# Kernel tuning notes

Measured on AMD Instinct MI355X. Metric: run time of the kernel, lower is better.

Reference implementation:

```python
import jax, jax.numpy as jnp
import numpy as np

# ---- module hyperparameters ----
B, L, F = 128, 720, 128
SEG = 24            # segment_length
NSEG = L // SEG     # 30 input segments
WIN = 15            # window_size
NPRED = 96 // SEG   # 4 prediction segments
D = 128             # encode_dim
H = 512             # hidden_dim
DECAY = 0.9
C = 1.0             # curvature
EPS = 1e-6
MAXN = 1.0 - 1e-5   # max radius of Poincare ball (c=1)
SQC = 1.0           # sqrt(C)

# ---- Poincare-ball manifold ops ----
def _sqnorm(x):
    return jnp.sum(x * x, axis=-1, keepdims=True)

def _norm(x):
    return jnp.sqrt(jnp.maximum(_sqnorm(x), EPS * EPS))

def _project(x):
    n = _norm(x)
    return jnp.where(n > MAXN, x * (MAXN / n), x)

def _artanh(x):
    return jnp.arctanh(jnp.clip(x, -1.0 + 1e-7, 1.0 - 1e-7))

def mobius_add(x, y):
    xy = jnp.sum(x * y, axis=-1, keepdims=True)
    x2, y2 = _sqnorm(x), _sqnorm(y)
    num = (1.0 + 2.0 * C * xy + C * y2) * x + (1.0 - C * x2) * y
    den = 1.0 + 2.0 * C * xy + C * C * x2 * y2
    return num / jnp.maximum(den, EPS)

def expmap0(v):
    n = _norm(v)
    return _project(jnp.tanh(SQC * n) * v / (SQC * n))

def logmap0(y):
    n = _norm(y)
    return _artanh(SQC * n) * y / (SQC * n)

def expmap(x, v):
    lam = 2.0 / jnp.maximum(1.0 - C * _sqnorm(x), EPS)
    n = _norm(v)
    second = jnp.tanh(SQC * lam * n / 2.0) * v / (SQC * n)
    return _project(mobius_add(x, second))

def logmap(x, y):
    d = mobius_add(-x, y)
    n = _norm(d)
    lam = 2.0 / jnp.maximum(1.0 - C * _sqnorm(x), EPS)
    return (2.0 / (SQC * lam)) * _artanh(SQC * n) * d / n


def setup_inputs() -> dict:
    key = jax.random.key(0)
    ks = jax.random.split(key, 12)
    s = 0.05
    return {
        'trend':           0.5 * jax.random.normal(ks[0], (B, L, F), jnp.float32),
        'seasonal_coarse': 0.5 * jax.random.normal(ks[1], (B, L, F), jnp.float32),
        'seasonal_fine':   0.5 * jax.random.normal(ks[2], (B, L, F), jnp.float32),
        'residual':        0.5 * jax.random.normal(ks[3], (B, L, F), jnp.float32),
        'W_t': s * jax.random.normal(ks[4], (SEG, D), jnp.float32), 'b_t': jnp.zeros((D,), jnp.float32),
        'W_c': s * jax.random.normal(ks[5], (SEG, D), jnp.float32), 'b_c': jnp.zeros((D,), jnp.float32),
        'W_f': s * jax.random.normal(ks[6], (SEG, D), jnp.float32), 'b_f': jnp.zeros((D,), jnp.float32),
        'W_r': s * jax.random.normal(ks[7], (SEG, D), jnp.float32), 'b_r': jnp.zeros((D,), jnp.float32),
        'alpha': jnp.array([0.5], jnp.float32),
        'W1': s * jax.random.normal(ks[8], (D, H), jnp.float32), 'b1': jnp.zeros((H,), jnp.float32),
        'W2': s * jax.random.normal(ks[9], (H, SEG), jnp.float32), 'b2': jnp.zeros((SEG,), jnp.float32),
    }


def reference(trend, seasonal_coarse, seasonal_fine, residual,
              W_t, b_t, W_c, b_c, W_f, b_f, W_r, b_r,
              alpha, W1, b1, W2, b2):
    b, l, f = trend.shape

    def collapse(x):  # [B,L,F] -> [B*F, NSEG, SEG]
        return x.transpose(0, 2, 1).reshape(b * f, NSEG, SEG)

    t_s, c_s, f_s, r_s = map(collapse, (trend, seasonal_coarse, seasonal_fine, residual))

    # per-segment tangent encoding (channel-independent, shared params)
    tan = (jnp.einsum('bns,sd->bnd', t_s, W_t) + b_t
           + jnp.einsum('bns,sd->bnd', c_s, W_c) + b_c
           + jnp.einsum('bns,sd->bnd', f_s, W_f) + b_f
           + jnp.einsum('bns,sd->bnd', r_s, W_r) + b_r)
    z = expmap0(tan)                     # [BF, NSEG, D] on the ball
    z_cur = z[:, -WIN:, :]

    idx = jnp.arange(WIN - 1, dtype=jnp.float32)
    w = DECAY ** (WIN - 2 - idx)
    w = w / w.sum()

    preds, latents = [], []
    for _ in range(NPRED):
        z_last = z_cur[:, -1]
        vel = logmap(z_cur[:, :-1], z_cur[:, 1:])
        avg_v = jnp.sum(vel * w[None, :, None], axis=1)    # [BF, D]
        z_next = expmap(z_last, alpha * avg_v)             # dynamics step
        latents.append(z_next)
        # reconstruction head: logmap0 -> MLP -> segment
        t0 = logmap0(z_next)
        seg = jax.nn.relu(t0 @ W1 + b1) @ W2 + b2          # [BF, SEG]
        preds.append(seg)
        z_cur = jnp.concatenate([z_cur[:, 1:], z_next[:, None]], axis=1)

    p = jnp.stack(preds, axis=1).reshape(b * f, NPRED * SEG)
    predictions = p.reshape(b, f, NPRED * SEG).transpose(0, 2, 1)  # [B, pred_len, F]
    return predictions
```

## Files before the change

kernel.cpp:

```cpp
#include <hip/hip_runtime.h>
#include <hip/hip_bf16.h>

namespace {
constexpr int kL = 720, kF = 128;
constexpr int kWin = 15;
constexpr float kEps = 1e-6f;
constexpr float kMaxN = 1.0f - 1e-5f;
constexpr int kT0off = 360;
constexpr int ZTR = 132;
constexpr int AROW = 104;
constexpr int XR = 129;
constexpr size_t kOffT0   = 0;
constexpr size_t kOffW1   = 16777216;
constexpr size_t kOffW2   = kOffW1 + 131072;
constexpr size_t kOffBt   = kOffW2 + 32768;
constexpr size_t kOffBsum = kOffBt + 73728;
constexpr size_t kOffZ2   = 17018880;
constexpr size_t kOffZ    = 18874368;
constexpr size_t kWsNew   = kOffZ + 125829120;
}

typedef float f32x4 __attribute__((ext_vector_type(4)));
typedef short s16x8 __attribute__((ext_vector_type(8)));

__device__ __forceinline__ float rcp_f(float x) { return __builtin_amdgcn_rcpf(x); }
__device__ __forceinline__ float sqrt_f(float x) { return __builtin_amdgcn_sqrtf(x); }
__device__ __forceinline__ float tanh_f(float x) {
  float t = __builtin_amdgcn_exp2f(x * -2.8853900817779268f);
  return (1.0f - t) * rcp_f(1.0f + t);
}
__device__ __forceinline__ float artanh_f(float n) {
  float nc = fminf(n, 1.0f - 1e-7f);
  return 0.34657359027997264f * __builtin_amdgcn_logf((1.0f + nc) * rcp_f(1.0f - nc));
}

template<int CTRL>
__device__ __forceinline__ float dpp_add(float v) {
  int mv = __builtin_amdgcn_update_dpp(0, __float_as_int(v), CTRL, 0xF, 0xF, false);
  return v + __int_as_float(mv);
}
__device__ __forceinline__ float sum16(float v) {
  v = dpp_add<0xB1>(v);
  v = dpp_add<0x4E>(v);
  v = dpp_add<0x141>(v);
  v = dpp_add<0x128>(v);
  return v;
}
__device__ __forceinline__ float sum64(float v) {
  v = sum16(v);
  v += __shfl_xor(v, 16);
  v += __shfl_xor(v, 32);
  return v;
}
__device__ __forceinline__ float rlane(float v, int i) {
  return __int_as_float(__builtin_amdgcn_readlane(__float_as_int(v), i));
}
__device__ __forceinline__ unsigned short rne_bf16(float f, float& fval) {
  unsigned u = __float_as_uint(f);
  unsigned r = (u + 0x7FFFu + ((u >> 16) & 1u)) & 0xFFFF0000u;
  fval = __uint_as_float(r);
  return (unsigned short)(r >> 16);
}

extern "C" __global__ __launch_bounds__(256)
void mwhf_prep(const float* __restrict__ W1, const float* __restrict__ W2,
               const float* __restrict__ W_t, const float* __restrict__ W_c,
               const float* __restrict__ W_f, const float* __restrict__ W_r,
               const float* __restrict__ b_t, const float* __restrict__ b_c,
               const float* __restrict__ b_f, const float* __restrict__ b_r,
               __hip_bfloat16* __restrict__ W1bf, __hip_bfloat16* __restrict__ W2bf,
               __hip_bfloat16* __restrict__ BtH, __hip_bfloat16* __restrict__ BtM,
               __hip_bfloat16* __restrict__ BtL, float* __restrict__ bsum)
{
  const int b = blockIdx.x, tid = threadIdx.x;
  if (b < 64) {
    const int n0 = b * 8;
    for (int e = tid; e < 1024; e += 256) {
      int n_l = e & 7, k = e >> 3;
      W1bf[(size_t)(n0 + n_l) * 128 + k] = __float2bfloat16(W1[(size_t)k * 512 + n0 + n_l]);
    }
  } else if (b < 68) {
    const int k0 = (b - 64) * 128;
    for (int e = tid; e < 4096; e += 256) {
      int p = e >> 7, k_l = e & 127;
      float v = (p < 24) ? W2[(size_t)(k0 + k_l) * 24 + p] : 0.0f;
      W2bf[(size_t)p * 512 + k0 + k_l] = __float2bfloat16(v);
    }
  } else if (b < 72) {
    const int st = b - 68;
    const float* src = (st == 0) ? W_t : (st == 1) ? W_c : (st == 2) ? W_f : W_r;
    for (int e = tid; e < 3072; e += 256) {
      int s = e >> 7, d = e & 127;
      float x = src[e];
      __hip_bfloat16 h = __float2bfloat16(x);
      float r1 = x - __bfloat162float(h);
      __hip_bfloat16 m = __float2bfloat16(r1);
      float r2 = r1 - __bfloat162float(m);
      const int o = d * 96 + st * 24 + s;
      BtH[o] = h;
      BtM[o] = m;
      BtL[o] = __float2bfloat16(r2);
    }
  } else {
    if (tid < 128) bsum[tid] = b_t[tid] + b_c[tid] + b_f[tid] + b_r[tid];
  }
}

extern "C" __global__ __launch_bounds__(256, 3)
void mwhf_k1a2(const float* __restrict__ trend,
               const float* __restrict__ seas_c,
               const float* __restrict__ seas_f,
               const float* __restrict__ resid,
               const __hip_bfloat16* __restrict__ BtH,
               const __hip_bfloat16* __restrict__ BtM,
               const __hip_bfloat16* __restrict__ BtL,
               const float* __restrict__ bsum,
               float* __restrict__ z_ws, float* __restrict__ z2_ws)
{
  __shared__ __align__(16) float X[96 * XR];

  const int tid = threadIdx.x;
  const int seg = blockIdx.x;
  const int bb  = blockIdx.y;

  {
    const float* ptrs[4] = {trend, seas_c, seas_f, resid};
#pragma unroll
    for (int it = 0; it < 12; ++it) {
      int e = it * 256 + tid;
      int row = e >> 5;
      int fq = (e & 31) * 4;
      int st = row / 24, sI = row - st * 24;
      float4 v = *(const float4*)&ptrs[st][(size_t)(bb * kL + kT0off + seg * 24 + sI) * kF + fq];
      float* dst = &X[row * XR + fq];
      dst[0] = v.x; dst[1] = v.y; dst[2] = v.z; dst[3] = v.w;
    }
  }
  __syncthreads();

  const int w = tid >> 6, lane = tid & 63;
  const int l16 = lane & 15, quad = lane >> 4;
  const int fbase = w * 32;

  f32x4 acc[2][8];
#pragma unroll
  for (int s = 0; s < 2; ++s)
#pragma unroll
    for (int t = 0; t < 8; ++t) acc[s][t] = (f32x4)0.f;

  const __hip_bfloat16* bhp = BtH + l16 * 96 + quad * 8;
  const __hip_bfloat16* bmp = BtM + l16 * 96 + quad * 8;
  const __hip_bfloat16* blp = BtL + l16 * 96 + quad * 8;

#pragma unroll
  for (int ks = 0; ks < 3; ++ks) {
    s16x8 ah[2], am[2], al[2];
#pragma unroll
    for (int s = 0; s < 2; ++s) {
      const int f = fbase + s * 16 + l16;
      const float* ar = &X[(ks * 32 + quad * 8) * XR + f];
#pragma unroll
      for (int j = 0; j < 8; ++j) {
        float x = ar[j * XR];
        unsigned hu = __float_as_uint(x) & 0xFFFF0000u;
        float r1 = x - __uint_as_float(hu);
        float mf; unsigned short mb = rne_bf16(r1, mf);
        float r2 = r1 - mf;
        float lf; unsigned short lb = rne_bf16(r2, lf);
        (void)lf;
        ah[s][j] = (short)(hu >> 16);
        am[s][j] = (short)mb;
        al[s][j] = (short)lb;
      }
    }
#pragma unroll
    for (int t = 0; t < 8; ++t) {
      s16x8 bh = *(const s16x8*)(bhp + t * 1536 + ks * 32);
      s16x8 bm = *(const s16x8*)(bmp + t * 1536 + ks * 32);
      s16x8 bl = *(const s16x8*)(blp + t * 1536 + ks * 32);
#pragma unroll
      for (int s = 0; s < 2; ++s) {
        acc[s][t] = __builtin_amdgcn_mfma_f32_16x16x32_bf16(ah[s], bh, acc[s][t], 0, 0, 0);
        acc[s][t] = __builtin_amdgcn_mfma_f32_16x16x32_bf16(am[s], bh, acc[s][t], 0, 0, 0);
        acc[s][t] = __builtin_amdgcn_mfma_f32_16x16x32_bf16(ah[s], bm, acc[s][t], 0, 0, 0);
        acc[s][t] = __builtin_amdgcn_mfma_f32_16x16x32_bf16(al[s], bh, acc[s][t], 0, 0, 0);
        acc[s][t] = __builtin_amdgcn_mfma_f32_16x16x32_bf16(ah[s], bl, acc[s][t], 0, 0, 0);
        acc[s][t] = __builtin_amdgcn_mfma_f32_16x16x32_bf16(am[s], bm, acc[s][t], 0, 0, 0);
      }
    }
  }

  float part[2][4] = {{0.f,0.f,0.f,0.f},{0.f,0.f,0.f,0.f}};
#pragma unroll
  for (int t = 0; t < 8; ++t) {
    float bv = bsum[t * 16 + l16];
#pragma unroll
    for (int s = 0; s < 2; ++s)
#pragma unroll
      for (int r = 0; r < 4; ++r) {
        float v = acc[s][t][r] + bv;
        acc[s][t][r] = v;
        part[s][r] += v * v;
      }
  }
#pragma unroll
  for (int s = 0; s < 2; ++s)
#pragma unroll
    for (int r = 0; r < 4; ++r) part[s][r] = sum16(part[s][r]);

#pragma unroll
  for (int s = 0; s < 2; ++s)
#pragma unroll
    for (int r = 0; r < 4; ++r) {
      const int f = fbase + s * 16 + quad * 4 + r;
      float v2 = part[s][r];
      float nv = sqrt_f(fmaxf(v2, 1e-12f));
      float sc = tanh_f(nv) * rcp_f(nv);
      float y2 = sc * sc * v2;
      float yn = sqrt_f(fmaxf(y2, 1e-12f));
      float proj = (yn > kMaxN) ? (kMaxN * rcp_f(yn)) : 1.0f;
      float scl = sc * proj;
      float* zr = z_ws + (size_t)(bb * 128 + f) * 1920 + seg * 128;
#pragma unroll
      for (int t = 0; t < 8; ++t)
        zr[t * 16 + l16] = acc[s][t][r] * scl;
      if (l16 == 0) z2_ws[(bb * 128 + f) * 16 + seg] = y2 * proj * proj;
    }
}

extern "C" __global__ __launch_bounds__(256, 6)
void mwhf_k1b(const float* __restrict__ z_ws, const float* __restrict__ z2_ws,
              const float* __restrict__ alpha,
              __hip_bfloat16* __restrict__ t0_out)
{
  __shared__ float z2s[80];
  __shared__ float pds[80];
  const int tid = threadIdx.x;
  const int w = tid >> 6, l = tid & 63;
  const int ro = blockIdx.x * 4 + w;

  float zx[19], zy[19];
  const float* zr = z_ws + (size_t)ro * 1920;
#pragma unroll
  for (int j = 0; j < 15; ++j) {
    float2 v = *(const float2*)&zr[j * 128 + 2 * l];
    zx[j] = v.x; zy[j] = v.y;
  }
  if (l < 15) z2s[w * 20 + l] = z2_ws[ro * 16 + l];

  {
    float pd[14];
#pragma unroll
    for (int j = 0; j < 14; ++j) pd[j] = zx[j] * zx[j + 1] + zy[j] * zy[j + 1];
#pragma unroll
    for (int j = 0; j < 14; ++j) pd[j] = sum64(pd[j]);
    if (l == 0) {
#pragma unroll
      for (int j = 0; j < 14; ++j) pds[w * 20 + j] = pd[j];
    }
  }

  const float alp = alpha[0];
  const float cw14 = (l < 14)
      ? __builtin_amdgcn_exp2f((float)(13 - l) * -0.15200309344504997f) * 0.12966260f
      : 0.f;

#pragma unroll
  for (int it = 0; it < 4; ++it) {
    float cA = 0.f, cB = 0.f, cW = 0.f;
    if (l < 14) {
      float dp = pds[w * 20 + it + l];
      float x2 = z2s[w * 20 + it + l];
      float y2 = z2s[w * 20 + it + l + 1];
      cA = 1.f - 2.f * dp + y2;
      cB = 1.f - x2;
      float den = fmaxf(1.f - 2.f * dp + x2 * y2, kEps);
      float invd = rcp_f(den);
      float d2 = (cA * cA * x2 - 2.f * cA * cB * dp + cB * cB * y2) * (invd * invd);
      float n = sqrt_f(fmaxf(d2, 1e-12f));
      float coef = fmaxf(cB, kEps) * artanh_f(n) * rcp_f(n);
      cW = cw14 * coef * invd;
    }
    float avx = 0.f, avy = 0.f;
#pragma unroll
    for (int i = 0; i < 14; ++i) {
      float sA = rlane(cA, i), sB = rlane(cB, i), sW = rlane(cW, i);
      float tx = sB * zx[it + i + 1] - sA * zx[it + i];
      float ty = sB * zy[it + i + 1] - sA * zy[it + i];
      avx += sW * tx;
      avy += sW * ty;
    }
    float vx = alp * avx, vy = alp * avy;
    const int pl = it + 14;
    float x2l = z2s[w * 20 + pl];
    float v2 = vx * vx + vy * vy;
    float xdv = zx[pl] * vx + zy[pl] * vy;
    v2 = sum64(v2);
    xdv = sum64(xdv);
    float nv = sqrt_f(fmaxf(v2, 1e-12f));
    float lam = 2.f * rcp_f(fmaxf(1.f - x2l, kEps));
    float co = tanh_f(0.5f * lam * nv) * rcp_f(nv);
    float s2 = co * co * v2;
    float xy = co * xdv;
    float P = 1.f + 2.f * xy + s2;
    float Q = 1.f - x2l;
    float den2 = fmaxf(1.f + 2.f * xy + x2l * s2, kEps);
    float invd2 = rcp_f(den2);
    float znx = (P * zx[pl] + Q * co * vx) * invd2;
    float zny = (P * zy[pl] + Q * co * vy) * invd2;
    float zn2 = (P * P * x2l + 2.f * P * Q * xy + Q * Q * s2) * (invd2 * invd2);
    float pdn = (P * x2l + Q * xy) * invd2;
    float yn = sqrt_f(fmaxf(zn2, 1e-12f));
    float proj = (yn > kMaxN) ? (kMaxN * rcp_f(yn)) : 1.f;
    znx *= proj; zny *= proj;
    zn2 *= proj * proj;
    pdn *= proj;
    zx[15 + it] = znx; zy[15 + it] = zny;
    if (l == 0) {
      z2s[w * 20 + 15 + it] = zn2;
      pds[w * 20 + 14 + it] = pdn;
    }
    float n0 = sqrt_f(fmaxf(zn2, 1e-12f));
    float fac = artanh_f(n0) * rcp_f(n0);
    __hip_bfloat162 hv;
    hv.x = __float2bfloat16(fac * znx);
    hv.y = __float2bfloat16(fac * zny);
    *(__hip_bfloat162*)(t0_out + ((size_t)ro * 4 + it) * 128 + 2 * l) = hv;
  }
}

extern "C" __global__ __launch_bounds__(256, 4)
void mwhf_k1(const float* __restrict__ trend,
             const float* __restrict__ seas_c,
             const float* __restrict__ seas_f,
             const float* __restrict__ resid,
             const __hip_bfloat16* __restrict__ BtH,
             const __hip_bfloat16* __restrict__ BtM,
             const __hip_bfloat16* __restrict__ BtL,
             const float* __restrict__ bsum,
             const float* __restrict__ alpha,
             __hip_bfloat16* __restrict__ t0_out)
{
  __shared__ __align__(16) char smem_raw[3 * 64 * AROW * 2];
  __shared__ float z2s[80];
  __shared__ float pds[80];

  float* ublk = (float*)smem_raw;
  __hip_bfloat16* Ah = (__hip_bfloat16*)smem_raw;
  __hip_bfloat16* Am = Ah + 64 * AROW;
  __hip_bfloat16* Al = Am + 64 * AROW;

  const int tid = threadIdx.x;
  const int bix = blockIdx.x;
  const int bb = (bix & 7) * 16 + (bix >> 8);
  const int f0 = ((bix >> 3) & 31) * 4;
  const int row0 = bb * 128 + f0;

  for (int e = tid; e < 192; e += 256) {
    int rr = e / 48, cc = e - rr * 48;
    int off = (rr * 16 + 15) * AROW;
    ((unsigned int*)(Ah + off))[cc] = 0u;
    ((unsigned int*)(Am + off))[cc] = 0u;
    ((unsigned int*)(Al + off))[cc] = 0u;
  }
  {
    const float* ptrs[4] = {trend, seas_c, seas_f, resid};
    for (int e = tid; e < 1440; e += 256) {
      int seg = e / 96;
      int k = e - seg * 96;
      int st = k / 24, s = k - st * 24;
      const float* p = ptrs[st];
      float4 v = *(const float4*)&p[(size_t)(bb * kL + kT0off + seg * 24 + s) * kF + f0];
      float xv[4] = {v.x, v.y, v.z, v.w};
#pragma unroll
      for (int f = 0; f < 4; ++f) {
        int m = f * 16 + seg;
        __hip_bfloat16 h = __float2bfloat16(xv[f]);
        float r1 = xv[f] - __bfloat162float(h);
        __hip_bfloat16 mm = __float2bfloat16(r1);
        float r2 = r1 - __bfloat162float(mm);
        Ah[m * AROW + k] = h;
        Am[m * AROW + k] = mm;
        Al[m * AROW + k] = __float2bfloat16(r2);
      }
    }
  }
  __syncthreads();

  const int w = tid >> 6;
  const int lane = tid & 63;
  const int l16 = lane & 15, quad = lane >> 4;

  f32x4 acc0[8];
  float scale4[4], zz4[4];
  {
    s16x8 ah[3], am[3], al[3];
    const int abase = (w * 16 + l16) * AROW + quad * 8;
#pragma unroll
    for (int ks = 0; ks < 3; ++ks) {
      ah[ks] = *(const s16x8*)(Ah + abase + ks * 32);
      am[ks] = *(const s16x8*)(Am + abase + ks * 32);
      al[ks] = *(const s16x8*)(Al + abase + ks * 32);
    }
#pragma unroll
    for (int t = 0; t < 8; ++t) acc0[t] = (f32x4)0.f;
    const __hip_bfloat16* bhp = BtH + l16 * 96 + quad * 8;
    const __hip_bfloat16* bmp = BtM + l16 * 96 + quad * 8;
    const __hip_bfloat16* blp = BtL + l16 * 96 + quad * 8;
#pragma unroll
    for (int t = 0; t < 8; ++t) {
#pragma unroll
      for (int ks = 0; ks < 3; ++ks) {
        s16x8 bh = *(const s16x8*)(bhp + t * 1536 + ks * 32);
        s16x8 bm = *(const s16x8*)(bmp + t * 1536 + ks * 32);
        s16x8 bl = *(const s16x8*)(blp + t * 1536 + ks * 32);
        acc0[t] = __builtin_amdgcn_mfma_f32_16x16x32_bf16(ah[ks], bh, acc0[t], 0, 0, 0);
        acc0[t] = __builtin_amdgcn_mfma_f32_16x16x32_bf16(am[ks], bh, acc0[t], 0, 0, 0);
        acc0[t] = __builtin_amdgcn_mfma_f32_16x16x32_bf16(ah[ks], bm, acc0[t], 0, 0, 0);
        acc0[t] = __builtin_amdgcn_mfma_f32_16x16x32_bf16(al[ks], bh, acc0[t], 0, 0, 0);
        acc0[t] = __builtin_amdgcn_mfma_f32_16x16x32_bf16(ah[ks], bl, acc0[t], 0, 0, 0);
        acc0[t] = __builtin_amdgcn_mfma_f32_16x16x32_bf16(am[ks], bm, acc0[t], 0, 0, 0);
      }
    }
    float part[4] = {0.f, 0.f, 0.f, 0.f};
#pragma unroll
    for (int t = 0; t < 8; ++t) {
      float bv = bsum[t * 16 + l16];
#pragma unroll
      for (int r = 0; r < 4; ++r) {
        float v = acc0[t][r] + bv;
        acc0[t][r] = v;
        part[r] += v * v;
      }
    }
#pragma unroll
    for (int r = 0; r < 4; ++r) part[r] = sum16(part[r]);
#pragma unroll
    for (int r = 0; r < 4; ++r) {
      float v2 = part[r];
      float nv = sqrt_f(fmaxf(v2, 1e-12f));
      float sc = tanh_f(nv) * rcp_f(nv);
      float y2 = sc * sc * v2;
      float yn = sqrt_f(fmaxf(y2, 1e-12f));
      float proj = (yn > kMaxN) ? (kMaxN * rcp_f(yn)) : 1.0f;
      scale4[r] = sc * proj;
      zz4[r] = y2 * proj * proj;
    }
  }
  __syncthreads();
  {
#pragma unroll
    for (int r = 0; r < 4; ++r) {
      int row = quad * 4 + r;
      if (row < kWin) {
#pragma unroll
        for (int t = 0; t < 8; ++t)
          ublk[(w * kWin + row) * ZTR + t * 16 + l16] = acc0[t][r] * scale4[r];
        if (l16 == 0) z2s[w * 20 + row] = zz4[r];
      }
    }
  }
  __syncthreads();

  {
    const int l = lane;
    float zx[19], zy[19];
#pragma unroll
    for (int j = 0; j < 15; ++j) {
      float2 v = *(const float2*)&ublk[(w * kWin + j) * ZTR + 2 * l];
      zx[j] = v.x; zy[j] = v.y;
    }
    {
      float pd[14];
#pragma unroll
      for (int j = 0; j < 14; ++j) pd[j] = zx[j] * zx[j + 1] + zy[j] * zy[j + 1];
#pragma unroll
      for (int j = 0; j < 14; ++j) pd[j] = sum64(pd[j]);
      if (l == 0) {
#pragma unroll
        for (int j = 0; j < 14; ++j) pds[w * 20 + j] = pd[j];
      }
    }
    const float alp = alpha[0];
    const float cw14 = (l < 14)
        ? __builtin_amdgcn_exp2f((float)(13 - l) * -0.15200309344504997f) * 0.12966260f
        : 0.f;
#pragma unroll
    for (int it = 0; it < 4; ++it) {
      float cA = 0.f, cB = 0.f, cW = 0.f;
      if (l < 14) {
        float dp = pds[w * 20 + it + l];
        float x2 = z2s[w * 20 + it + l];
        float y2 = z2s[w * 20 + it + l + 1];
        cA = 1.f - 2.f * dp + y2;
        cB = 1.f - x2;
        float den = fmaxf(1.f - 2.f * dp + x2 * y2, kEps);
        float invd = rcp_f(den);
        float d2 = (cA * cA * x2 - 2.f * cA * cB * dp + cB * cB * y2) * (invd * invd);
        float n = sqrt_f(fmaxf(d2, 1e-12f));
        float coef = fmaxf(cB, kEps) * artanh_f(n) * rcp_f(n);
        cW = cw14 * coef * invd;
      }
      float avx = 0.f, avy = 0.f;
#pragma unroll
      for (int i = 0; i < 14; ++i) {
        float sA = rlane(cA, i), sB = rlane(cB, i), sW = rlane(cW, i);
        float tx = sB * zx[it + i + 1] - sA * zx[it + i];
        float ty = sB * zy[it + i + 1] - sA * zy[it + i];
        avx += sW * tx;
        avy += sW * ty;
      }
      float vx = alp * avx, vy = alp * avy;
      const int pl = it + 14;
      float x2l = z2s[w * 20 + pl];
      float v2 = vx * vx + vy * vy;
      float xdv = zx[pl] * vx + zy[pl] * vy;
      v2 = sum64(v2);
      xdv = sum64(xdv);
      float nv = sqrt_f(fmaxf(v2, 1e-12f));
      float lam = 2.f * rcp_f(fmaxf(1.f - x2l, kEps));
      float co = tanh_f(0.5f * lam * nv) * rcp_f(nv);
      float s2 = co * co * v2;
      float xy = co * xdv;
      float P = 1.f + 2.f * xy + s2;
      float Q = 1.f - x2l;
      float den2 = fmaxf(1.f + 2.f * xy + x2l * s2, kEps);
      float invd2 = rcp_f(den2);
      float znx = (P * zx[pl] + Q * co * vx) * invd2;
      float zny = (P * zy[pl] + Q * co * vy) * invd2;
      float zn2 = (P * P * x2l + 2.f * P * Q * xy + Q * Q * s2) * (invd2 * invd2);
      float pdn = (P * x2l + Q * xy) * invd2;
      float yn = sqrt_f(fmaxf(zn2, 1e-12f));
      float proj = (yn > kMaxN) ? (kMaxN * rcp_f(yn)) : 1.f;
      znx *= proj; zny *= proj;
      zn2 *= proj * proj;
      pdn *= proj;
      zx[15 + it] = znx; zy[15 + it] = zny;
      if (l == 0) {
        z2s[w * 20 + 15 + it] = zn2;
        pds[w * 20 + 14 + it] = pdn;
      }
      float n0 = sqrt_f(fmaxf(zn2, 1e-12f));
      float fac = artanh_f(n0) * rcp_f(n0);
      __hip_bfloat162 hv;
      hv.x = __float2bfloat16(fac * znx);
      hv.y = __float2bfloat16(fac * zny);
      *(__hip_bfloat162*)(t0_out + ((size_t)(row0 + w) * 4 + it) * 128 + 2 * l) = hv;
    }
  }
}

extern "C" __global__ __launch_bounds__(256, 4)
void mwhf_k2g(const __hip_bfloat16* __restrict__ t0g,
              const __hip_bfloat16* __restrict__ W1bf,
              const __hip_bfloat16* __restrict__ W2bf,
              const float* __restrict__ b1, const float* __restrict__ b2,
              float* __restrict__ outp)
{
  __shared__ __align__(16) __hip_bfloat16 hids[32 * 512];
  s16x8* hidv = (s16x8*)hids;

  const int tid = threadIdx.x;
  const int w = tid >> 6, lane = tid & 63;
  const int l16 = lane & 15, quad = lane >> 4;
  const int mbase = blockIdx.x * 32;
  const int ng = w * 128;

  s16x8 afr[2][4];
#pragma unroll
  for (int s = 0; s < 2; ++s)
#pragma unroll
    for (int kc = 0; kc < 4; ++kc)
      afr[s][kc] = *(const s16x8*)(t0g + (size_t)(mbase + s * 16 + l16) * 128 + kc * 32 + quad * 8);

  f32x4 acc[2][8];
#pragma unroll
  for (int s = 0; s < 2; ++s)
#pragma unroll
    for (int t = 0; t < 8; ++t) acc[s][t] = (f32x4)0.f;

#pragma unroll
  for (int t = 0; t < 8; ++t) {
    const __hip_bfloat16* bp = W1bf + (size_t)(ng + t * 16 + l16) * 128 + quad * 8;
#pragma unroll
    for (int kc = 0; kc < 4; ++kc) {
      s16x8 bfr = *(const s16x8*)(bp + kc * 32);
      acc[0][t] = __builtin_amdgcn_mfma_f32_16x16x32_bf16(afr[0][kc], bfr, acc[0][t], 0, 0, 0);
      acc[1][t] = __builtin_amdgcn_mfma_f32_16x16x32_bf16(afr[1][kc], bfr, acc[1][t], 0, 0, 0);
    }
  }
#pragma unroll
  for (int t = 0; t < 8; ++t) {
    const int nl = ng + t * 16 + l16;
    float bv = b1[nl];
#pragma unroll
    for (int s = 0; s < 2; ++s)
#pragma unroll
      for (int r = 0; r < 4; ++r) {
        int m = s * 16 + quad * 4 + r;
// ... 14 lines not shown
      a2 = __builtin_amdgcn_mfma_f32_16x16x32_bf16(av, bfr, a2, 0, 0, 0);
    }
    const int p = t2 * 16 + l16;
    if (p < 24) {
      float bv = b2[p];
#pragma unroll
      for (int r = 0; r < 4; ++r) {
        int m = mbase + s2i * 16 + quad * 4 + r;
        int bbi = m >> 9, it = m & 3, f = (m >> 2) & 127;
        outp[(size_t)bbi * 12288 + (it * 24 + p) * 128 + f] = a2[r] + bv;
      }
    }
  }
}

extern "C" void kernel_launch(void* const* d_in, const int* in_sizes, int n_in,
                              void* d_out, int out_size, void* d_ws, size_t ws_size,
                              hipStream_t stream) {
  (void)in_sizes; (void)n_in; (void)out_size;
  const float* trend = (const float*)d_in[0];
  const float* sc    = (const float*)d_in[1];
  const float* sf    = (const float*)d_in[2];
  const float* rs    = (const float*)d_in[3];
  const float* W_t   = (const float*)d_in[4];
  const float* b_t   = (const float*)d_in[5];
  const float* W_c   = (const float*)d_in[6];
  const float* b_c   = (const float*)d_in[7];
  const float* W_f   = (const float*)d_in[8];
  const float* b_f   = (const float*)d_in[9];
  const float* W_r   = (const float*)d_in[10];
  const float* b_r   = (const float*)d_in[11];
  const float* alpha = (const float*)d_in[12];
  const float* W1    = (const float*)d_in[13];
  const float* b1    = (const float*)d_in[14];
  const float* W2    = (const float*)d_in[15];
  const float* b2    = (const float*)d_in[16];

  char* ws = (char*)d_ws;
  __hip_bfloat16* t0   = (__hip_bfloat16*)(ws + kOffT0);
  __hip_bfloat16* W1bf = (__hip_bfloat16*)(ws + kOffW1);
  __hip_bfloat16* W2bf = (__hip_bfloat16*)(ws + kOffW2);
  __hip_bfloat16* BtH  = (__hip_bfloat16*)(ws + kOffBt);
  __hip_bfloat16* BtM  = BtH + 12288;
  __hip_bfloat16* BtL  = BtM + 12288;
  float* bsum = (float*)(ws + kOffBsum);
  float* z2w  = (float*)(ws + kOffZ2);
  float* zw   = (float*)(ws + kOffZ);
  float* outp = (float*)d_out;

  hipLaunchKernelGGL(mwhf_prep, dim3(73), dim3(256), 0, stream,
                     W1, W2, W_t, W_c, W_f, W_r, b_t, b_c, b_f, b_r,
                     W1bf, W2bf, BtH, BtM, BtL, bsum);
  if (ws_size >= kWsNew) {
    hipLaunchKernelGGL(mwhf_k1a2, dim3(15, 128), dim3(256), 0, stream,
                       trend, sc, sf, rs, BtH, BtM, BtL, bsum, zw, z2w);
    hipLaunchKernelGGL(mwhf_k1b, dim3(4096), dim3(256), 0, stream,
                       zw, z2w, alpha, t0);
  } else {
    hipLaunchKernelGGL(mwhf_k1, dim3(4096), dim3(256), 0, stream,
                       trend, sc, sf, rs, BtH, BtM, BtL, bsum, alpha, t0);
  }
  hipLaunchKernelGGL(mwhf_k2g, dim3(2048), dim3(256), 0, stream,
                     t0, W1bf, W2bf, b1, b2, outp);
}
```

Measured before the change: 374.8 us.

## Fuse dynamics step with MLP head and split encoder blocks by feature half

The dynamics kernel now also runs the reconstruction MLP. It keeps the 32 t0 rows per block in swizzled shared memory, so the t0 round trip through global memory and one kernel launch go away. The encoder kernel is split across feature halves: twice as many blocks, each with half the shared memory and accumulators, and launch bounds raised to allow more blocks per CU. The fused kernel uses 512 threads and more shared memory per block, which may lower occupancy.

```diff
diff --git a/kernel.cpp b/kernel.cpp
--- a/kernel.cpp
+++ b/kernel.cpp
@@ -9,7 +9,7 @@
 constexpr int kT0off = 360;
 constexpr int ZTR = 132;
 constexpr int AROW = 104;
-constexpr int XR = 129;
+constexpr int XR2 = 65;
 constexpr size_t kOffT0   = 0;
 constexpr size_t kOffW1   = 16777216;
 constexpr size_t kOffW2   = kOffW1 + 131072;
@@ -106,8 +106,8 @@
   }
 }
 
-extern "C" __global__ __launch_bounds__(256, 3)
-void mwhf_k1a2(const float* __restrict__ trend,
+extern "C" __global__ __launch_bounds__(256, 4)
+void mwhf_k1a3(const float* __restrict__ trend,
                const float* __restrict__ seas_c,
                const float* __restrict__ seas_f,
                const float* __restrict__ resid,
@@ -117,22 +117,24 @@
                const float* __restrict__ bsum,
                float* __restrict__ z_ws, float* __restrict__ z2_ws)
 {
-  __shared__ __align__(16) float X[96 * XR];
+  __shared__ __align__(16) float X[96 * XR2];
 
   const int tid = threadIdx.x;
   const int seg = blockIdx.x;
-  const int bb  = blockIdx.y;
+  const int bh  = blockIdx.y;
+  const int bb  = bh >> 1;
+  const int fh  = (bh & 1) * 64;
 
   {
     const float* ptrs[4] = {trend, seas_c, seas_f, resid};
 #pragma unroll
-    for (int it = 0; it < 12; ++it) {
+    for (int it = 0; it < 6; ++it) {
       int e = it * 256 + tid;
-      int row = e >> 5;
-      int fq = (e & 31) * 4;
+      int row = e >> 4;
+      int fq = (e & 15) * 4;
       int st = row / 24, sI = row - st * 24;
-      float4 v = *(const float4*)&ptrs[st][(size_t)(bb * kL + kT0off + seg * 24 + sI) * kF + fq];
-      float* dst = &X[row * XR + fq];
+      float4 v = *(const float4*)&ptrs[st][(size_t)(bb * kL + kT0off + seg * 24 + sI) * kF + fh + fq];
+      float* dst = &X[row * XR2 + fq];
       dst[0] = v.x; dst[1] = v.y; dst[2] = v.z; dst[3] = v.w;
     }
   }
@@ -140,13 +142,10 @@
 
   const int w = tid >> 6, lane = tid & 63;
   const int l16 = lane & 15, quad = lane >> 4;
-  const int fbase = w * 32;
-
-  f32x4 acc[2][8];
-#pragma unroll
-  for (int s = 0; s < 2; ++s)
-#pragma unroll
-    for (int t = 0; t < 8; ++t) acc[s][t] = (f32x4)0.f;
+
+  f32x4 acc[8];
+#pragma unroll
+  for (int t = 0; t < 8; ++t) acc[t] = (f32x4)0.f;
 
   const __hip_bfloat16* bhp = BtH + l16 * 96 + quad * 8;
   const __hip_bfloat16* bmp = BtM + l16 * 96 + quad * 8;
@@ -154,322 +153,99 @@
 
 #pragma unroll
   for (int ks = 0; ks < 3; ++ks) {
-    s16x8 ah[2], am[2], al[2];
-#pragma unroll
-    for (int s = 0; s < 2; ++s) {
-      const int f = fbase + s * 16 + l16;
-      const float* ar = &X[(ks * 32 + quad * 8) * XR + f];
+    s16x8 ah, am, al;
+    {
+      const float* ar = &X[(ks * 32 + quad * 8) * XR2 + w * 16 + l16];
 #pragma unroll
       for (int j = 0; j < 8; ++j) {
-        float x = ar[j * XR];
+        float x = ar[j * XR2];
         unsigned hu = __float_as_uint(x) & 0xFFFF0000u;
         float r1 = x - __uint_as_float(hu);
         float mf; unsigned short mb = rne_bf16(r1, mf);
         float r2 = r1 - mf;
         float lf; unsigned short lb = rne_bf16(r2, lf);
         (void)lf;
-        ah[s][j] = (short)(hu >> 16);
-        am[s][j] = (short)mb;
-        al[s][j] = (short)lb;
+        ah[j] = (short)(hu >> 16);
+        am[j] = (short)mb;
+        al[j] = (short)lb;
       }
     }
 #pragma unroll
     for (int t = 0; t < 8; ++t) {
-      s16x8 bh = *(const s16x8*)(bhp + t * 1536 + ks * 32);
-      s16x8 bm = *(const s16x8*)(bmp + t * 1536 + ks * 32);
-      s16x8 bl = *(const s16x8*)(blp + t * 1536 + ks * 32);
-#pragma unroll
-      for (int s = 0; s < 2; ++s) {
-        acc[s][t] = __builtin_amdgcn_mfma_f32_16x16x32_bf16(ah[s], bh, acc[s][t], 0, 0, 0);
-        acc[s][t] = __builtin_amdgcn_mfma_f32_16x16x32_bf16(am[s], bh, acc[s][t], 0, 0, 0);
-        acc[s][t] = __builtin_amdgcn_mfma_f32_16x16x32_bf16(ah[s], bm, acc[s][t], 0, 0, 0);
-        acc[s][t] = __builtin_amdgcn_mfma_f32_16x16x32_bf16(al[s], bh, acc[s][t], 0, 0, 0);
-        acc[s][t] = __builtin_amdgcn_mfma_f32_16x16x32_bf16(ah[s], bl, acc[s][t], 0, 0, 0);
-        acc[s][t] = __builtin_amdgcn_mfma_f32_16x16x32_bf16(am[s], bm, acc[s][t], 0, 0, 0);
-      }
-    }
-  }
-
-  float part[2][4] = {{0.f,0.f,0.f,0.f},{0.f,0.f,0.f,0.f}};
+      s16x8 bhv = *(const s16x8*)(bhp + t * 1536 + ks * 32);
+      s16x8 bmv = *(const s16x8*)(bmp + t * 1536 + ks * 32);
+      s16x8 blv = *(const s16x8*)(blp + t * 1536 + ks * 32);
+      acc[t] = __builtin_amdgcn_mfma_f32_16x16x32_bf16(ah, bhv, acc[t], 0, 0, 0);
+      acc[t] = __builtin_amdgcn_mfma_f32_16x16x32_bf16(am, bhv, acc[t], 0, 0, 0);
+      acc[t] = __builtin_amdgcn_mfma_f32_16x16x32_bf16(ah, bmv, acc[t], 0, 0, 0);
+      acc[t] = __builtin_amdgcn_mfma_f32_16x16x32_bf16(al, bhv, acc[t], 0, 0, 0);
+      acc[t] = __builtin_amdgcn_mfma_f32_16x16x32_bf16(ah, blv, acc[t], 0, 0, 0);
+      acc[t] = __builtin_amdgcn_mfma_f32_16x16x32_bf16(am, bmv, acc[t], 0, 0, 0);
+    }
+  }
+
+  float part[4] = {0.f, 0.f, 0.f, 0.f};
 #pragma unroll
   for (int t = 0; t < 8; ++t) {
     float bv = bsum[t * 16 + l16];
 #pragma unroll
-    for (int s = 0; s < 2; ++s)
-#pragma unroll
-      for (int r = 0; r < 4; ++r) {
-        float v = acc[s][t][r] + bv;
-        acc[s][t][r] = v;
-        part[s][r] += v * v;
-      }
-  }
-#pragma unroll
-  for (int s = 0; s < 2; ++s)
-#pragma unroll
-    for (int r = 0; r < 4; ++r) part[s][r] = sum16(part[s][r]);
-
-#pragma unroll
-  for (int s = 0; s < 2; ++s)
-#pragma unroll
     for (int r = 0; r < 4; ++r) {
-      const int f = fbase + s * 16 + quad * 4 + r;
-      float v2 = part[s][r];
-      float nv = sqrt_f(fmaxf(v2, 1e-12f));
-      float sc = tanh_f(nv) * rcp_f(nv);
-      float y2 = sc * sc * v2;
-      float yn = sqrt_f(fmaxf(y2, 1e-12f));
-      float proj = (yn > kMaxN) ? (kMaxN * rcp_f(yn)) : 1.0f;
-      float scl = sc * proj;
-      float* zr = z_ws + (size_t)(bb * 128 + f) * 1920 + seg * 128;
-#pragma unroll
-      for (int t = 0; t < 8; ++t)
-        zr[t * 16 + l16] = acc[s][t][r] * scl;
-      if (l16 == 0) z2_ws[(bb * 128 + f) * 16 + seg] = y2 * proj * proj;
-    }
-}
-
-extern "C" __global__ __launch_bounds__(256, 6)
-void mwhf_k1b(const float* __restrict__ z_ws, const float* __restrict__ z2_ws,
-              const float* __restrict__ alpha,
-              __hip_bfloat16* __restrict__ t0_out)
+      float v = acc[t][r] + bv;
+      acc[t][r] = v;
+      part[r] += v * v;
+    }
+  }
+#pragma unroll
+  for (int r = 0; r < 4; ++r) part[r] = sum16(part[r]);
+
+#pragma unroll
+  for (int r = 0; r < 4; ++r) {
+    const int row = bh * 64 + w * 16 + quad * 4 + r;
+    float v2 = part[r];
+    float nv = sqrt_f(fmaxf(v2, 1e-12f));
+    float sc = tanh_f(nv) * rcp_f(nv);
+    float y2 = sc * sc * v2;
+    float yn = sqrt_f(fmaxf(y2, 1e-12f));
+    float proj = (yn > kMaxN) ? (kMaxN * rcp_f(yn)) : 1.0f;
+    float scl = sc * proj;
+    float* zr = z_ws + (size_t)row * 1920 + seg * 128;
+#pragma unroll
+    for (int t = 0; t < 8; ++t)
+      zr[t * 16 + l16] = acc[t][r] * scl;
+    if (l16 == 0) z2_ws[row * 16 + seg] = y2 * proj * proj;
+  }
+}
+
+extern "C" __global__ __launch_bounds__(512, 4)
+void mwhf_k1bg(const float* __restrict__ z_ws, const float* __restrict__ z2_ws,
+               const float* __restrict__ alpha,
+               const __hip_bfloat16* __restrict__ W1bf,
+               const __hip_bfloat16* __restrict__ W2bf,
+               const float* __restrict__ b1, const float* __restrict__ b2,
+               float* __restrict__ outp)
 {
-  __shared__ float z2s[80];
-  __shared__ float pds[80];
+  __shared__ __align__(16) __hip_bfloat16 t0s[32 * 128];
+  __shared__ __align__(16) __hip_bfloat16 hids[32 * 512];
+  __shared__ float z2s[160];
+  __shared__ float pds[160];
+  s16x8* hidv = (s16x8*)hids;
+
   const int tid = threadIdx.x;
   const int w = tid >> 6, l = tid & 63;
-  const int ro = blockIdx.x * 4 + w;
-
-  float zx[19], zy[19];
-  const float* zr = z_ws + (size_t)ro * 1920;
-#pragma unroll
-  for (int j = 0; j < 15; ++j) {
-    float2 v = *(const float2*)&zr[j * 128 + 2 * l];
-    zx[j] = v.x; zy[j] = v.y;
-  }
-  if (l < 15) z2s[w * 20 + l] = z2_ws[ro * 16 + l];
+  const int l16 = l & 15, quad = l >> 4;
+  const int mbase = blockIdx.x * 32;
 
   {
-    float pd[14];
-#pragma unroll
-    for (int j = 0; j < 14; ++j) pd[j] = zx[j] * zx[j + 1] + zy[j] * zy[j + 1];
-#pragma unroll
-    for (int j = 0; j < 14; ++j) pd[j] = sum64(pd[j]);
-    if (l == 0) {
-#pragma unroll
-      for (int j = 0; j < 14; ++j) pds[w * 20 + j] = pd[j];
-    }
-  }
-
-  const float alp = alpha[0];
-  const float cw14 = (l < 14)
-      ? __builtin_amdgcn_exp2f((float)(13 - l) * -0.15200309344504997f) * 0.12966260f
-      : 0.f;
-
-#pragma unroll
-  for (int it = 0; it < 4; ++it) {
-    float cA = 0.f, cB = 0.f, cW = 0.f;
-    if (l < 14) {
-      float dp = pds[w * 20 + it + l];
-      float x2 = z2s[w * 20 + it + l];
-      float y2 = z2s[w * 20 + it + l + 1];
-      cA = 1.f - 2.f * dp + y2;
-      cB = 1.f - x2;
-      float den = fmaxf(1.f - 2.f * dp + x2 * y2, kEps);
-      float invd = rcp_f(den);
-      float d2 = (cA * cA * x2 - 2.f * cA * cB * dp + cB * cB * y2) * (invd * invd);
-      float n = sqrt_f(fmaxf(d2, 1e-12f));
-      float coef = fmaxf(cB, kEps) * artanh_f(n) * rcp_f(n);
-      cW = cw14 * coef * invd;
-    }
-    float avx = 0.f, avy = 0.f;
-#pragma unroll
-    for (int i = 0; i < 14; ++i) {
-      float sA = rlane(cA, i), sB = rlane(cB, i), sW = rlane(cW, i);
-      float tx = sB * zx[it + i + 1] - sA * zx[it + i];
-      float ty = sB * zy[it + i + 1] - sA * zy[it + i];
-      avx += sW * tx;
-      avy += sW * ty;
-    }
-    float vx = alp * avx, vy = alp * avy;
-    const int pl = it + 14;
-    float x2l = z2s[w * 20 + pl];
-    float v2 = vx * vx + vy * vy;
-    float xdv = zx[pl] * vx + zy[pl] * vy;
-    v2 = sum64(v2);
-    xdv = sum64(xdv);
-    float nv = sqrt_f(fmaxf(v2, 1e-12f));
-    float lam = 2.f * rcp_f(fmaxf(1.f - x2l, kEps));
-    float co = tanh_f(0.5f * lam * nv) * rcp_f(nv);
-    float s2 = co * co * v2;
-    float xy = co * xdv;
-    float P = 1.f + 2.f * xy + s2;
-    float Q = 1.f - x2l;
-    float den2 = fmaxf(1.f + 2.f * xy + x2l * s2, kEps);
-    float invd2 = rcp_f(den2);
-    float znx = (P * zx[pl] + Q * co * vx) * invd2;
-    float zny = (P * zy[pl] + Q * co * vy) * invd2;
-    float zn2 = (P * P * x2l + 2.f * P * Q * xy + Q * Q * s2) * (invd2 * invd2);
-    float pdn = (P * x2l + Q * xy) * invd2;
-    float yn = sqrt_f(fmaxf(zn2, 1e-12f));
-    float proj = (yn > kMaxN) ? (kMaxN * rcp_f(yn)) : 1.f;
-    znx *= proj; zny *= proj;
-    zn2 *= proj * proj;
-    pdn *= proj;
-    zx[15 + it] = znx; zy[15 + it] = zny;
-    if (l == 0) {
-      z2s[w * 20 + 15 + it] = zn2;
-      pds[w * 20 + 14 + it] = pdn;
-    }
-    float n0 = sqrt_f(fmaxf(zn2, 1e-12f));
-    float fac = artanh_f(n0) * rcp_f(n0);
-    __hip_bfloat162 hv;
-    hv.x = __float2bfloat16(fac * znx);
-    hv.y = __float2bfloat16(fac * zny);
-    *(__hip_bfloat162*)(t0_out + ((size_t)ro * 4 + it) * 128 + 2 * l) = hv;
-  }
-}
-
-extern "C" __global__ __launch_bounds__(256, 4)
-void mwhf_k1(const float* __restrict__ trend,
-             const float* __restrict__ seas_c,
-             const float* __restrict__ seas_f,
-             const float* __restrict__ resid,
-             const __hip_bfloat16* __restrict__ BtH,
-             const __hip_bfloat16* __restrict__ BtM,
-             const __hip_bfloat16* __restrict__ BtL,
-             const float* __restrict__ bsum,
-             const float* __restrict__ alpha,
-             __hip_bfloat16* __restrict__ t0_out)
-{
-  __shared__ __align__(16) char smem_raw[3 * 64 * AROW * 2];
-  __shared__ float z2s[80];
-  __shared__ float pds[80];
-
-  float* ublk = (float*)smem_raw;
-  __hip_bfloat16* Ah = (__hip_bfloat16*)smem_raw;
-  __hip_bfloat16* Am = Ah + 64 * AROW;
-  __hip_bfloat16* Al = Am + 64 * AROW;
-
-  const int tid = threadIdx.x;
-  const int bix = blockIdx.x;
-  const int bb = (bix & 7) * 16 + (bix >> 8);
-  const int f0 = ((bix >> 3) & 31) * 4;
-  const int row0 = bb * 128 + f0;
-
-  for (int e = tid; e < 192; e += 256) {
-    int rr = e / 48, cc = e - rr * 48;
-    int off = (rr * 16 + 15) * AROW;
-    ((unsigned int*)(Ah + off))[cc] = 0u;
-    ((unsigned int*)(Am + off))[cc] = 0u;
-    ((unsigned int*)(Al + off))[cc] = 0u;
-  }
-  {
-    const float* ptrs[4] = {trend, seas_c, seas_f, resid};
-    for (int e = tid; e < 1440; e += 256) {
-      int seg = e / 96;
-      int k = e - seg * 96;
-      int st = k / 24, s = k - st * 24;
-      const float* p = ptrs[st];
-      float4 v = *(const float4*)&p[(size_t)(bb * kL + kT0off + seg * 24 + s) * kF + f0];
-      float xv[4] = {v.x, v.y, v.z, v.w};
-#pragma unroll
-      for (int f = 0; f < 4; ++f) {
-        int m = f * 16 + seg;
-        __hip_bfloat16 h = __float2bfloat16(xv[f]);
-        float r1 = xv[f] - __bfloat162float(h);
-        __hip_bfloat16 mm = __float2bfloat16(r1);
-        float r2 = r1 - __bfloat162float(mm);
-        Ah[m * AROW + k] = h;
-        Am[m * AROW + k] = mm;
-        Al[m * AROW + k] = __float2bfloat16(r2);
-      }
-    }
-  }
-  __syncthreads();
-
-  const int w = tid >> 6;
-  const int lane = tid & 63;
-  const int l16 = lane & 15, quad = lane >> 4;
-
-  f32x4 acc0[8];
-  float scale4[4], zz4[4];
-  {
-    s16x8 ah[3], am[3], al[3];
-    const int abase = (w * 16 + l16) * AROW + quad * 8;
-#pragma unroll
-    for (int ks = 0; ks < 3; ++ks) {
-      ah[ks] = *(const s16x8*)(Ah + abase + ks * 32);
-      am[ks] = *(const s16x8*)(Am + abase + ks * 32);
-      al[ks] = *(const s16x8*)(Al + abase + ks * 32);
-    }
-#pragma unroll
-    for (int t = 0; t < 8; ++t) acc0[t] = (f32x4)0.f;
-    const __hip_bfloat16* bhp = BtH + l16 * 96 + quad * 8;
-    const __hip_bfloat16* bmp = BtM + l16 * 96 + quad * 8;
-    const __hip_bfloat16* blp = BtL + l16 * 96 + quad * 8;
-#pragma unroll
-    for (int t = 0; t < 8; ++t) {
-#pragma unroll
-      for (int ks = 0; ks < 3; ++ks) {
-        s16x8 bh = *(const s16x8*)(bhp + t * 1536 + ks * 32);
-        s16x8 bm = *(const s16x8*)(bmp + t * 1536 + ks * 32);
-        s16x8 bl = *(const s16x8*)(blp + t * 1536 + ks * 32);
-        acc0[t] = __builtin_amdgcn_mfma_f32_16x16x32_bf16(ah[ks], bh, acc0[t], 0, 0, 0);
-        acc0[t] = __builtin_amdgcn_mfma_f32_16x16x32_bf16(am[ks], bh, acc0[t], 0, 0, 0);
-        acc0[t] = __builtin_amdgcn_mfma_f32_16x16x32_bf16(ah[ks], bm, acc0[t], 0, 0, 0);
-        acc0[t] = __builtin_amdgcn_mfma_f32_16x16x32_bf16(al[ks], bh, acc0[t], 0, 0, 0);
-        acc0[t] = __builtin_amdgcn_mfma_f32_16x16x32_bf16(ah[ks], bl, acc0[t], 0, 0, 0);
-        acc0[t] = __builtin_amdgcn_mfma_f32_16x16x32_bf16(am[ks], bm, acc0[t], 0, 0, 0);
-      }
-    }
-    float part[4] = {0.f, 0.f, 0.f, 0.f};
-#pragma unroll
-    for (int t = 0; t < 8; ++t) {
-      float bv = bsum[t * 16 + l16];
-#pragma unroll
-      for (int r = 0; r < 4; ++r) {
-        float v = acc0[t][r] + bv;
-        acc0[t][r] = v;
-        part[r] += v * v;
-      }
-    }
-#pragma unroll
-    for (int r = 0; r < 4; ++r) part[r] = sum16(part[r]);
-#pragma unroll
-    for (int r = 0; r < 4; ++r) {
-      float v2 = part[r];
-      float nv = sqrt_f(fmaxf(v2, 1e-12f));
-      float sc = tanh_f(nv) * rcp_f(nv);
-      float y2 = sc * sc * v2;
-      float yn = sqrt_f(fmaxf(y2, 1e-12f));
-      float proj = (yn > kMaxN) ? (kMaxN * rcp_f(yn)) : 1.0f;
-      scale4[r] = sc * proj;
-      zz4[r] = y2 * proj * proj;
-    }
-  }
-  __syncthreads();
-  {
-#pragma unroll
-    for (int r = 0; r < 4; ++r) {
-      int row = quad * 4 + r;
-      if (row < kWin) {
-#pragma unroll
-        for (int t = 0; t < 8; ++t)
-          ublk[(w * kWin + row) * ZTR + t * 16 + l16] = acc0[t][r] * scale4[r];
-        if (l16 == 0) z2s[w * 20 + row] = zz4[r];
-      }
-    }
-  }
-  __syncthreads();
-
-  {
-    const int l = lane;
+    const int ro = blockIdx.x * 8 + w;
     float zx[19], zy[19];
+    const float* zr = z_ws + (size_t)ro * 1920;
 #pragma unroll
     for (int j = 0; j < 15; ++j) {
-      float2 v = *(const float2*)&ublk[(w * kWin + j) * ZTR + 2 * l];
+      float2 v = *(const float2*)&zr[j * 128 + 2 * l];
       zx[j] = v.x; zy[j] = v.y;
     }
+    if (l < 15) z2s[w * 20 + l] = z2_ws[ro * 16 + l];
+
     {
       float pd[14];
 #pragma unroll
@@ -481,10 +257,12 @@
         for (int j = 0; j < 14; ++j) pds[w * 20 + j] = pd[j];
       }
     }
+
     const float alp = alpha[0];
     const float cw14 = (l < 14)
         ? __builtin_amdgcn_exp2f((float)(13 - l) * -0.15200309344504997f) * 0.12966260f
         : 0.f;
+
 #pragma unroll
     for (int it = 0; it < 4; ++it) {
       float cA = 0.f, cB = 0.f, cW = 0.f;
@@ -545,6 +323,294 @@
       __hip_bfloat162 hv;
       hv.x = __float2bfloat16(fac * znx);
       hv.y = __float2bfloat16(fac * zny);
+      const int mloc = w * 4 + it;
+      const int cs = (2 * l) ^ ((mloc & 7) << 3);
+      *(__hip_bfloat162*)&t0s[mloc * 128 + cs] = hv;
+    }
+  }
+  __syncthreads();
+
+  {
+    const int ng = w * 64;
+    s16x8 afr[2][4];
+#pragma unroll
+    for (int s = 0; s < 2; ++s)
+#pragma unroll
+      for (int kc = 0; kc < 4; ++kc)
+        afr[s][kc] = *(const s16x8*)&t0s[(s * 16 + l16) * 128 +
+                                         ((kc * 32 + quad * 8) ^ ((l16 & 7) << 3))];
+
+    f32x4 acc2[2][4];
+#pragma unroll
+    for (int s = 0; s < 2; ++s)
+#pragma unroll
+      for (int t = 0; t < 4; ++t) acc2[s][t] = (f32x4)0.f;
+
+#pragma unroll
+    for (int t = 0; t < 4; ++t) {
+      const __hip_bfloat16* bp = W1bf + (size_t)(ng + t * 16 + l16) * 128 + quad * 8;
+#pragma unroll
+      for (int kc = 0; kc < 4; ++kc) {
+        s16x8 bfr = *(const s16x8*)(bp + kc * 32);
+        acc2[0][t] = __builtin_amdgcn_mfma_f32_16x16x32_bf16(afr[0][kc], bfr, acc2[0][t], 0, 0, 0);
+        acc2[1][t] = __builtin_amdgcn_mfma_f32_16x16x32_bf16(afr[1][kc], bfr, acc2[1][t], 0, 0, 0);
+      }
+    }
+#pragma unroll
+    for (int t = 0; t < 4; ++t) {
+      const int nl = ng + t * 16 + l16;
+      float bv = b1[nl];
+#pragma unroll
+      for (int s = 0; s < 2; ++s)
+#pragma unroll
+        for (int r = 0; r < 4; ++r) {
+          int m = s * 16 + quad * 4 + r;
+          float h = fmaxf(acc2[s][t][r] + bv, 0.f);
+          hids[m * 512 + (nl ^ ((m & 7) << 3))] = __float2bfloat16(h);
+        }
+    }
+  }
+  __syncthreads();
+
+  if (w < 4) {
+    const int s2i = w & 1, t2 = w >> 1;
+    f32x4 a2 = (f32x4)0.f;
+    const int mrow = s2i * 16 + l16;
+#pragma unroll 4
+    for (int kc = 0; kc < 16; ++kc) {
+      s16x8 av = hidv[mrow * 64 + ((kc * 4 + quad) ^ (l16 & 7))];
+      s16x8 bfr = *(const s16x8*)(W2bf + (size_t)(t2 * 16 + l16) * 512 + kc * 32 + quad * 8);
+      a2 = __builtin_amdgcn_mfma_f32_16x16x32_bf16(av, bfr, a2, 0, 0, 0);
+    }
+    const int p = t2 * 16 + l16;
+    if (p < 24) {
+      float bv = b2[p];
+#pragma unroll
+      for (int r = 0; r < 4; ++r) {
+        int m = mbase + s2i * 16 + quad * 4 + r;
+        int bbi = m >> 9, it = m & 3, f = (m >> 2) & 127;
+        outp[(size_t)bbi * 12288 + (it * 24 + p) * 128 + f] = a2[r] + bv;
+      }
+    }
+  }
+}
+
+extern "C" __global__ __launch_bounds__(256, 4)
+void mwhf_k1(const float* __restrict__ trend,
+             const float* __restrict__ seas_c,
+             const float* __restrict__ seas_f,
+             const float* __restrict__ resid,
+             const __hip_bfloat16* __restrict__ BtH,
+             const __hip_bfloat16* __restrict__ BtM,
+             const __hip_bfloat16* __restrict__ BtL,
+             const float* __restrict__ bsum,
+             const float* __restrict__ alpha,
+             __hip_bfloat16* __restrict__ t0_out)
+{
+  __shared__ __align__(16) char smem_raw[3 * 64 * AROW * 2];
+  __shared__ float z2s[80];
+  __shared__ float pds[80];
+
+  float* ublk = (float*)smem_raw;
+  __hip_bfloat16* Ah = (__hip_bfloat16*)smem_raw;
+  __hip_bfloat16* Am = Ah + 64 * AROW;
+  __hip_bfloat16* Al = Am + 64 * AROW;
+
+  const int tid = threadIdx.x;
+  const int bix = blockIdx.x;
+  const int bb = (bix & 7) * 16 + (bix >> 8);
+  const int f0 = ((bix >> 3) & 31) * 4;
+  const int row0 = bb * 128 + f0;
+
+  for (int e = tid; e < 192; e += 256) {
+    int rr = e / 48, cc = e - rr * 48;
+    int off = (rr * 16 + 15) * AROW;
+    ((unsigned int*)(Ah + off))[cc] = 0u;
+    ((unsigned int*)(Am + off))[cc] = 0u;
+    ((unsigned int*)(Al + off))[cc] = 0u;
+  }
+  {
+    const float* ptrs[4] = {trend, seas_c, seas_f, resid};
+    for (int e = tid; e < 1440; e += 256) {
+      int seg = e / 96;
+      int k = e - seg * 96;
+      int st = k / 24, s = k - st * 24;
+      const float* p = ptrs[st];
+      float4 v = *(const float4*)&p[(size_t)(bb * kL + kT0off + seg * 24 + s) * kF + f0];
+      float xv[4] = {v.x, v.y, v.z, v.w};
+#pragma unroll
+      for (int f = 0; f < 4; ++f) {
+        int m = f * 16 + seg;
+        __hip_bfloat16 h = __float2bfloat16(xv[f]);
+        float r1 = xv[f] - __bfloat162float(h);
+        __hip_bfloat16 mm = __float2bfloat16(r1);
+        float r2 = r1 - __bfloat162float(mm);
+        Ah[m * AROW + k] = h;
+        Am[m * AROW + k] = mm;
+        Al[m * AROW + k] = __float2bfloat16(r2);
+      }
+    }
+  }
+  __syncthreads();
+
+  const int w = tid >> 6;
+  const int lane = tid & 63;
+  const int l16 = lane & 15, quad = lane >> 4;
+
+  f32x4 acc0[8];
+  float scale4[4], zz4[4];
+  {
+    s16x8 ah[3], am[3], al[3];
+    const int abase = (w * 16 + l16) * AROW + quad * 8;
+#pragma unroll
+    for (int ks = 0; ks < 3; ++ks) {
+      ah[ks] = *(const s16x8*)(Ah + abase + ks * 32);
+      am[ks] = *(const s16x8*)(Am + abase + ks * 32);
+      al[ks] = *(const s16x8*)(Al + abase + ks * 32);
+    }
+#pragma unroll
+    for (int t = 0; t < 8; ++t) acc0[t] = (f32x4)0.f;
+    const __hip_bfloat16* bhp = BtH + l16 * 96 + quad * 8;
+    const __hip_bfloat16* bmp = BtM + l16 * 96 + quad * 8;
+    const __hip_bfloat16* blp = BtL + l16 * 96 + quad * 8;
+#pragma unroll
+    for (int t = 0; t < 8; ++t) {
+#pragma unroll
+      for (int ks = 0; ks < 3; ++ks) {
+        s16x8 bh = *(const s16x8*)(bhp + t * 1536 + ks * 32);
+        s16x8 bm = *(const s16x8*)(bmp + t * 1536 + ks * 32);
+        s16x8 bl = *(const s16x8*)(blp + t * 1536 + ks * 32);
+        acc0[t] = __builtin_amdgcn_mfma_f32_16x16x32_bf16(ah[ks], bh, acc0[t], 0, 0, 0);
+        acc0[t] = __builtin_amdgcn_mfma_f32_16x16x32_bf16(am[ks], bh, acc0[t], 0, 0, 0);
+        acc0[t] = __builtin_amdgcn_mfma_f32_16x16x32_bf16(ah[ks], bm, acc0[t], 0, 0, 0);
+        acc0[t] = __builtin_amdgcn_mfma_f32_16x16x32_bf16(al[ks], bh, acc0[t], 0, 0, 0);
+        acc0[t] = __builtin_amdgcn_mfma_f32_16x16x32_bf16(ah[ks], bl, acc0[t], 0, 0, 0);
+        acc0[t] = __builtin_amdgcn_mfma_f32_16x16x32_bf16(am[ks], bm, acc0[t], 0, 0, 0);
+      }
+    }
+    float part[4] = {0.f, 0.f, 0.f, 0.f};
+#pragma unroll
+    for (int t = 0; t < 8; ++t) {
+      float bv = bsum[t * 16 + l16];
+#pragma unroll
+      for (int r = 0; r < 4; ++r) {
+        float v = acc0[t][r] + bv;
+        acc0[t][r] = v;
+        part[r] += v * v;
+      }
+    }
+#pragma unroll
+    for (int r = 0; r < 4; ++r) part[r] = sum16(part[r]);
+#pragma unroll
+    for (int r = 0; r < 4; ++r) {
+      float v2 = part[r];
+      float nv = sqrt_f(fmaxf(v2, 1e-12f));
+      float sc = tanh_f(nv) * rcp_f(nv);
+      float y2 = sc * sc * v2;
+      float yn = sqrt_f(fmaxf(y2, 1e-12f));
+      float proj = (yn > kMaxN) ? (kMaxN * rcp_f(yn)) : 1.0f;
+      scale4[r] = sc * proj;
+      zz4[r] = y2 * proj * proj;
+    }
+  }
+  __syncthreads();
+  {
+#pragma unroll
+    for (int r = 0; r < 4; ++r) {
+      int row = quad * 4 + r;
+      if (row < kWin) {
+#pragma unroll
+        for (int t = 0; t < 8; ++t)
+          ublk[(w * kWin + row) * ZTR + t * 16 + l16] = acc0[t][r] * scale4[r];
+        if (l16 == 0) z2s[w * 20 + row] = zz4[r];
+      }
+    }
+  }
+  __syncthreads();
+
+  {
+    const int l = lane;
+    float zx[19], zy[19];
+#pragma unroll
+    for (int j = 0; j < 15; ++j) {
+      float2 v = *(const float2*)&ublk[(w * kWin + j) * ZTR + 2 * l];
+      zx[j] = v.x; zy[j] = v.y;
+    }
+    {
+      float pd[14];
+#pragma unroll
+      for (int j = 0; j < 14; ++j) pd[j] = zx[j] * zx[j + 1] + zy[j] * zy[j + 1];
+#pragma unroll
+      for (int j = 0; j < 14; ++j) pd[j] = sum64(pd[j]);
+      if (l == 0) {
+#pragma unroll
+        for (int j = 0; j < 14; ++j) pds[w * 20 + j] = pd[j];
+      }
+    }
+    const float alp = alpha[0];
+    const float cw14 = (l < 14)
+        ? __builtin_amdgcn_exp2f((float)(13 - l) * -0.15200309344504997f) * 0.12966260f
+        : 0.f;
+#pragma unroll
+    for (int it = 0; it < 4; ++it) {
+      float cA = 0.f, cB = 0.f, cW = 0.f;
+      if (l < 14) {
+        float dp = pds[w * 20 + it + l];
+        float x2 = z2s[w * 20 + it + l];
+        float y2 = z2s[w * 20 + it + l + 1];
+        cA = 1.f - 2.f * dp + y2;
+        cB = 1.f - x2;
+        float den = fmaxf(1.f - 2.f * dp + x2 * y2, kEps);
+        float invd = rcp_f(den);
+        float d2 = (cA * cA * x2 - 2.f * cA * cB * dp + cB * cB * y2) * (invd * invd);
+        float n = sqrt_f(fmaxf(d2, 1e-12f));
+        float coef = fmaxf(cB, kEps) * artanh_f(n) * rcp_f(n);
+        cW = cw14 * coef * invd;
+      }
+      float avx = 0.f, avy = 0.f;
+#pragma unroll
+      for (int i = 0; i < 14; ++i) {
+        float sA = rlane(cA, i), sB = rlane(cB, i), sW = rlane(cW, i);
+        float tx = sB * zx[it + i + 1] - sA * zx[it + i];
+        float ty = sB * zy[it + i + 1] - sA * zy[it + i];
+        avx += sW * tx;
+        avy += sW * ty;
+      }
+      float vx = alp * avx, vy = alp * avy;
+      const int pl = it + 14;
+      float x2l = z2s[w * 20 + pl];
+      float v2 = vx * vx + vy * vy;
+      float xdv = zx[pl] * vx + zy[pl] * vy;
+      v2 = sum64(v2);
+      xdv = sum64(xdv);
+      float nv = sqrt_f(fmaxf(v2, 1e-12f));
+      float lam = 2.f * rcp_f(fmaxf(1.f - x2l, kEps));
+      float co = tanh_f(0.5f * lam * nv) * rcp_f(nv);
+      float s2 = co * co * v2;
+      float xy = co * xdv;
+      float P = 1.f + 2.f * xy + s2;
+      float Q = 1.f - x2l;
+      float den2 = fmaxf(1.f + 2.f * xy + x2l * s2, kEps);
+      float invd2 = rcp_f(den2);
+      float znx = (P * zx[pl] + Q * co * vx) * invd2;
+      float zny = (P * zy[pl] + Q * co * vy) * invd2;
+      float zn2 = (P * P * x2l + 2.f * P * Q * xy + Q * Q * s2) * (invd2 * invd2);
+      float pdn = (P * x2l + Q * xy) * invd2;
+      float yn = sqrt_f(fmaxf(zn2, 1e-12f));
+      float proj = (yn > kMaxN) ? (kMaxN * rcp_f(yn)) : 1.f;
+      znx *= proj; zny *= proj;
+      zn2 *= proj * proj;
+      pdn *= proj;
+      zx[15 + it] = znx; zy[15 + it] = zny;
+      if (l == 0) {
+        z2s[w * 20 + 15 + it] = zn2;
+        pds[w * 20 + 14 + it] = pdn;
+      }
+      float n0 = sqrt_f(fmaxf(zn2, 1e-12f));
+      float fac = artanh_f(n0) * rcp_f(n0);
+      __hip_bfloat162 hv;
+      hv.x = __float2bfloat16(fac * znx);
+      hv.y = __float2bfloat16(fac * zny);
       *(__hip_bfloat162*)(t0_out + ((size_t)(row0 + w) * 4 + it) * 128 + 2 * l) = hv;
     }
   }
@@ -665,14 +731,14 @@
                      W1, W2, W_t, W_c, W_f, W_r, b_t, b_c, b_f, b_r,
                      W1bf, W2bf, BtH, BtM, BtL, bsum);
   if (ws_size >= kWsNew) {
-    hipLaunchKernelGGL(mwhf_k1a2, dim3(15, 128), dim3(256), 0, stream,
+    hipLaunchKernelGGL(mwhf_k1a3, dim3(15, 256), dim3(256), 0, stream,
                        trend, sc, sf, rs, BtH, BtM, BtL, bsum, zw, z2w);
-    hipLaunchKernelGGL(mwhf_k1b, dim3(4096), dim3(256), 0, stream,
-                       zw, z2w, alpha, t0);
+    hipLaunchKernelGGL(mwhf_k1bg, dim3(2048), dim3(512), 0, stream,
+                       zw, z2w, alpha, W1bf, W2bf, b1, b2, outp);
   } else {
     hipLaunchKernelGGL(mwhf_k1, dim3(4096), dim3(256), 0, stream,
                        trend, sc, sf, rs, BtH, BtM, BtL, bsum, alpha, t0);
-  }
-  hipLaunchKernelGGL(mwhf_k2g, dim3(2048), dim3(256), 0, stream,
-                     t0, W1bf, W2bf, b1, b2, outp);
-}
+    hipLaunchKernelGGL(mwhf_k2g, dim3(2048), dim3(256), 0, stream,
+                       t0, W1bf, W2bf, b1, b2, outp);
+  }
+}
```

Measured after the change: 349.5 us. 6.7% less time.
